# Kernel optimization log

Hardware: AMD Instinct MI355X
Metric: run time of the kernel (lower is better)

Reference implementation:

```python
import jax, jax.numpy as jnp
import numpy as np

B, H, S, D = 2, 16, 2048, 64
DEGREE = 2
EPS = 1e-4


def setup_inputs() -> dict:
    key = jax.random.key(0)
    kq, kk, kv = jax.random.split(key, 3)
    q = jax.random.normal(kq, (B, H, S, D), dtype=jnp.float32)
    k = jax.random.normal(kk, (B, H, S, D), dtype=jnp.float32)
    v = jax.random.normal(kv, (B, H, S, D), dtype=jnp.float32)
    return {"q": q, "k": k, "v": v}


def reference(q, k, v):
    # dots: [B,H,S,S] = QK^T
    dots = jnp.einsum("bhsd,bhtd->bhst", q, k)
    # polynomial kernel: x^degree, row-normalized with clamped denom
    x = dots ** DEGREE
    denom = jnp.maximum(x.sum(axis=-1, keepdims=True), EPS)
    attn = x / denom
    # weighted V sum: [B,H,S,D]
    return jnp.einsum("bhst,bhtd->bhsd", attn, v)
```

## Files before the change

### kernel.cpp

```cpp
#include <hip/hip_runtime.h>


#define S_LEN 2048
#define DH    64
#define BQ    64
#define BK    64
#define EPSTR 68
#define PSTR  65
#define BH_N  32
#define PER_BH (S_LEN * DH)
#define NT    (S_LEN / BK)

typedef __bf16 bf16x8 __attribute__((ext_vector_type(8)));
typedef __bf16 bf16x2 __attribute__((ext_vector_type(2)));
typedef float  f32x2  __attribute__((ext_vector_type(2)));
typedef float  f32x4  __attribute__((ext_vector_type(4)));
typedef float  f32x16 __attribute__((ext_vector_type(16)));
typedef unsigned int uivec2 __attribute__((ext_vector_type(2)));

__device__ __forceinline__ unsigned short f2bf(float f) {
    union { float f; unsigned int u; } x; x.f = f;
    unsigned int u = x.u;
    return (unsigned short)((u + 0x7fffu + ((u >> 16) & 1u)) >> 16);
}

__device__ __forceinline__ unsigned int pack2bf(float lo, float hi) {
#if __has_builtin(__builtin_amdgcn_cvt_pk_bf16_f32)
    bf16x2 p = __builtin_amdgcn_cvt_pk_bf16_f32(lo, hi);
    union { bf16x2 v; unsigned int u; } c; c.v = p;
    return c.u;
#else
    return (unsigned int)f2bf(lo) | ((unsigned int)f2bf(hi) << 16);
#endif
}

__device__ __forceinline__ void pl32swap(unsigned int& a, unsigned int& b) {
#if __has_builtin(__builtin_amdgcn_permlane32_swap)
    uivec2 r = __builtin_amdgcn_permlane32_swap(a, b, false, false);
    a = r[0]; b = r[1];
#else
    asm("v_permlane32_swap_b32 %0, %1" : "+v"(a), "+v"(b));
#endif
}

__global__ __launch_bounds__(256)
void prepass_kernel(const float* __restrict__ kg, const float* __restrict__ vg,
                    unsigned short* __restrict__ kfo, unsigned short* __restrict__ vfo)
{
    __shared__ unsigned short Lk[64 * 72];
    __shared__ unsigned short Lv[64 * PSTR];
    const int tid = threadIdx.x;
    const int bh  = blockIdx.y;
    const int t   = blockIdx.x;
    const size_t base = (size_t)bh * PER_BH + (size_t)t * 64 * DH;

    const float4* kf4 = (const float4*)(kg + base);
    const float4* vf4 = (const float4*)(vg + base);
    #pragma unroll
    for (int r = 0; r < 4; ++r) {
        int idx = r * 256 + tid;
        int row = idx >> 4, c4 = idx & 15;
        float4 f = kf4[idx];
        ushort4 hh;
        hh.x = f2bf(f.x); hh.y = f2bf(f.y); hh.z = f2bf(f.z); hh.w = f2bf(f.w);
        *(ushort4*)&Lk[row * 72 + c4 * 4] = hh;
        float4 g = vf4[idx];
        unsigned short* pv = &Lv[row * PSTR + c4 * 4];
        pv[0] = f2bf(g.x); pv[1] = f2bf(g.y); pv[2] = f2bf(g.z); pv[3] = f2bf(g.w);
    }
    __syncthreads();

    unsigned short* kout = kfo + (size_t)bh * PER_BH + (size_t)t * 4096;
    #pragma unroll
    for (int r = 0; r < 2; ++r) {
        int pos = r * 256 + tid;
        int lam = pos & 63, rest = pos >> 6;
        int e = rest >> 2, ks = rest & 3;
        int l31 = lam & 31, h = lam >> 5;
        uint4 v = *(const uint4*)&Lk[(e * 32 + l31) * 72 + ks * 16 + h * 8];
        *(uint4*)(kout + (size_t)pos * 8) = v;
    }
    unsigned short* vout = vfo + (size_t)bh * PER_BH + (size_t)t * 4096;
    #pragma unroll
    for (int r = 0; r < 2; ++r) {
        int pos = r * 256 + tid;
        int lam = pos & 63, rest = pos >> 6;
        int e = rest >> 2, ksl = (rest >> 1) & 1, mt = rest & 1;
        int l31 = lam & 31, h = lam >> 5;
        int d  = mt * 32 + l31;
        int j0 = e * 32 + ksl * 16 + h * 8;
        union { unsigned short s[8]; uint4 u; } u;
        #pragma unroll
        for (int jj = 0; jj < 8; ++jj) u.s[jj] = Lv[(j0 + jj) * PSTR + d];
        *(uint4*)(vout + (size_t)pos * 8) = u.u;
    }
}

__global__ __launch_bounds__(256, 3)
void poly_attn_main(const float* __restrict__ qg,
                    const unsigned short* __restrict__ kfo,
                    const unsigned short* __restrict__ vfo,
                    float* __restrict__ og)
{
    __shared__ float epb[4 * 32 * EPSTR];
    __shared__ float dbuf[128];

    const int tid  = threadIdx.x;
    const int lane = tid & 63;
    const int w    = tid >> 6;
    const int sp   = w >> 1;
    const int e    = w & 1;
    const int l31  = lane & 31;
    const int h    = lane >> 5;

    const int id = blockIdx.x;
    const int r5 = id & 31;
    const int bh = (r5 & 7) * 4 + (r5 >> 3);
    const int qt = id >> 5;
    const int q0 = qt * BQ;

    const float* qb = qg + ((size_t)bh * S_LEN + q0) * DH;
    const unsigned short* kw = kfo + (size_t)bh * PER_BH + e * 2048 + (size_t)lane * 8;
    const unsigned short* vw = vfo + (size_t)bh * PER_BH + e * 2048 + (size_t)lane * 8;
    float* ob = og + ((size_t)bh * S_LEN + q0) * DH;

    bf16x8 qfrag[4];
    #pragma unroll
    for (int ks = 0; ks < 4; ++ks) {
        const float* qp = qb + (32 * sp + l31) * DH + ks * 16 + h * 8;
        float4 f0 = *(const float4*)qp;
        float4 f1 = *(const float4*)(qp + 4);
        union { unsigned int d[4]; bf16x8 v; } u;
        u.d[0] = pack2bf(f0.x, f0.y);
        u.d[1] = pack2bf(f0.z, f0.w);
        u.d[2] = pack2bf(f1.x, f1.y);
        u.d[3] = pack2bf(f1.z, f1.w);
        qfrag[ks] = u.v;
    }

    f32x16 oacc[2];
    #pragma unroll
    for (int mt = 0; mt < 2; ++mt)
        #pragma unroll
        for (int r = 0; r < 16; ++r) oacc[mt][r] = 0.f;
    f32x16 oaccD;
    #pragma unroll
    for (int r = 0; r < 16; ++r) oaccD[r] = 0.f;

    f32x16 zacc;
    #pragma unroll
    for (int r = 0; r < 16; ++r) zacc[r] = 0.f;
    asm volatile("" : "+v"(zacc));

    bf16x8 onesv;
    {
        union { unsigned int d[4]; bf16x8 v; } u;
        u.d[0] = 0x3f803f80u; u.d[1] = 0x3f803f80u;
        u.d[2] = 0x3f803f80u; u.d[3] = 0x3f803f80u;
        onesv = u.v;
    }
    asm volatile("" : "+v"(onesv));

    uint4 kbuf[2][4], vbuf[4];
    unsigned int bsv[2][4];

    #pragma unroll
    for (int x = 0; x < 4; ++x) kbuf[0][x] = *(const uint4*)(kw + x * 512);

#define BODY(TT, CUR, NXT, KPF)                                                     \
    {                                                                               \
        {                                                                           \
            const unsigned short* vn_ = vw + (size_t)(TT) * 4096;                   \
            _Pragma("unroll")                                                       \
            for (int x = 0; x < 4; ++x) vbuf[x] = *(const uint4*)(vn_ + x * 512);   \
        }                                                                           \
        f32x16 acc;                                                                 \
        __builtin_amdgcn_s_setprio(1);                                              \
        {                                                                           \
            union { uint4 u; bf16x8 v; } kc;                                        \
            kc.u = kbuf[CUR][0];                                                    \
            acc = __builtin_amdgcn_mfma_f32_32x32x16_bf16(kc.v, qfrag[0], zacc, 0, 0, 0); \
            kc.u = kbuf[CUR][1];                                                    \
            acc = __builtin_amdgcn_mfma_f32_32x32x16_bf16(kc.v, qfrag[1], acc, 0, 0, 0); \
            kc.u = kbuf[CUR][2];                                                    \
            acc = __builtin_amdgcn_mfma_f32_32x32x16_bf16(kc.v, qfrag[2], acc, 0, 0, 0); \
            kc.u = kbuf[CUR][3];                                                    \
            acc = __builtin_amdgcn_mfma_f32_32x32x16_bf16(kc.v, qfrag[3], acc, 0, 0, 0); \
        }                                                                           \
        __builtin_amdgcn_s_setprio(0);                                              \
        if (KPF) {                                                                  \
            const unsigned short* kn_ = kw + (size_t)((TT) + 1) * 4096;             \
            _Pragma("unroll")                                                       \
            for (int x = 0; x < 4; ++x) kbuf[NXT][x] = *(const uint4*)(kn_ + x * 512); \
        }                                                                           \
        _Pragma("unroll")                                                           \
        for (int ksl = 0; ksl < 2; ++ksl) {                                         \
            f32x2 va, vb, vc, vd;                                                   \
            va[0] = acc[8*ksl+0]; va[1] = acc[8*ksl+1];                             \
            vb[0] = acc[8*ksl+2]; vb[1] = acc[8*ksl+3];                             \
            vc[0] = acc[8*ksl+4]; vc[1] = acc[8*ksl+5];                             \
            vd[0] = acc[8*ksl+6]; vd[1] = acc[8*ksl+7];                             \
            va = va * va; vb = vb * vb; vc = vc * vc; vd = vd * vd;                 \
            unsigned int a0 = pack2bf(va[0], va[1]);                                \
            unsigned int a1 = pack2bf(vb[0], vb[1]);                                \
            unsigned int b0 = pack2bf(vc[0], vc[1]);                                \
            unsigned int b1 = pack2bf(vd[0], vd[1]);                                \
            pl32swap(a0, b0);                                                       \
            pl32swap(a1, b1);                                                       \
            bsv[ksl][0] = a0; bsv[ksl][1] = a1;                                     \
            bsv[ksl][2] = b0; bsv[ksl][3] = b1;                                     \
        }                                                                           \
        __builtin_amdgcn_s_setprio(1);                                              \
        _Pragma("unroll")                                                           \
        for (int ksl = 0; ksl < 2; ++ksl) {                                         \
            union { unsigned int d[4]; bf16x8 v; } bu;                              \
            bu.d[0] = bsv[ksl][0]; bu.d[1] = bsv[ksl][1];                           \
            bu.d[2] = bsv[ksl][2]; bu.d[3] = bsv[ksl][3];                           \
            union { uint4 u; bf16x8 v; } vv;                                        \
            vv.u = vbuf[ksl * 2 + 0];                                               \
            oacc[0] = __builtin_amdgcn_mfma_f32_32x32x16_bf16(vv.v, bu.v, oacc[0], 0, 0, 0); \
            vv.u = vbuf[ksl * 2 + 1];                                               \
            oacc[1] = __builtin_amdgcn_mfma_f32_32x32x16_bf16(vv.v, bu.v, oacc[1], 0, 0, 0); \
            oaccD  = __builtin_amdgcn_mfma_f32_32x32x16_bf16(onesv, bu.v, oaccD, 0, 0, 0); \
        }                                                                           \
        __builtin_amdgcn_s_setprio(0);                                              \
    }

    for (int T = 0; T < NT - 2; T += 2) {
        BODY(T,     0, 1, 1);
        BODY(T + 1, 1, 0, 1);
    }
    BODY(NT - 2, 0, 1, 1);
    BODY(NT - 1, 1, 0, 0);
#undef BODY

    const float wavetot = oaccD[0];

    {
        float* ep = epb + (size_t)w * (32 * EPSTR);
        #pragma unroll
        for (int mt = 0; mt < 2; ++mt) {
            #pragma unroll
            for (int g = 0; g < 4; ++g) {
                f32x4 vv;
                vv[0] = oacc[mt][4*g+0];
                vv[1] = oacc[mt][4*g+1];
                vv[2] = oacc[mt][4*g+2];
                vv[3] = oacc[mt][4*g+3];
                *(f32x4*)&ep[l31 * EPSTR + mt * 32 + 8 * g + 4 * h] = vv;
            }
        }
        if (h == 0) dbuf[w * 32 + l31] = wavetot;
    }
    __syncthreads();

    const int so = w >> 1, ho = w & 1;
    const int lr = lane >> 1;
    const float den = dbuf[(2 * so + 0) * 32 + lr] + dbuf[(2 * so + 1) * 32 + lr];
    const float inv = 1.0f / fmaxf(den, 1e-4f);
    const float* ea = epb + (size_t)(2 * so + 0) * (32 * EPSTR) + lr * EPSTR;
    const float* eb = epb + (size_t)(2 * so + 1) * (32 * EPSTR) + lr * EPSTR;
    #pragma unroll
    for (int it = 0; it < 4; ++it) {
        int d0 = ho * 32 + (lane & 1) * 16 + it * 4;
        f32x4 a = *(const f32x4*)&ea[d0];
        f32x4 b = *(const f32x4*)&eb[d0];
        f32x4 sm;
        sm[0] = (a[0] + b[0]) * inv;
        sm[1] = (a[1] + b[1]) * inv;
        sm[2] = (a[2] + b[2]) * inv;
        sm[3] = (a[3] + b[3]) * inv;
        *(f32x4*)&ob[(32 * so + lr) * DH + d0] = sm;
    }
}

#define LSTR 72
__global__ __launch_bounds__(256, 2)
void poly_attn_fallback(const float* __restrict__ qg, const float* __restrict__ kg,
                        const float* __restrict__ vg, float* __restrict__ og)
{
    __shared__ unsigned short Qs[64 * LSTR];
    __shared__ unsigned short Ksl[64 * LSTR];
    __shared__ unsigned short Vt[64 * LSTR];
    __shared__ unsigned short Xsl[64 * LSTR];

    const int tid  = threadIdx.x;
    const int lane = tid & 63;
    const int w    = tid >> 6;
    const int c    = lane & 15;
    const int quad = lane >> 4;
    const int i0   = w * 16;

    const int bh = blockIdx.y;
    const int q0 = blockIdx.x * 64;

    const float* qb = qg + ((size_t)bh * S_LEN + q0) * DH;
    const float* kb = kg + (size_t)bh * S_LEN * DH;
    const float* vb = vg + (size_t)bh * S_LEN * DH;
    float*       ob = og + ((size_t)bh * S_LEN + q0) * DH;

    {
        const float4* qf4 = (const float4*)qb;
        #pragma unroll
        for (int r = 0; r < 4; ++r) {
            int idx = r * 256 + tid;
            int row = idx >> 4, c4 = idx & 15;
            float4 f = qf4[idx];
            ushort4 hh;
            hh.x = f2bf(f.x); hh.y = f2bf(f.y); hh.z = f2bf(f.z); hh.w = f2bf(f.w);
            *(ushort4*)&Qs[row * LSTR + c4 * 4] = hh;
        }
    }

    f32x4 oacc[4];
    #pragma unroll
    for (int t = 0; t < 4; ++t) { oacc[t][0]=0.f; oacc[t][1]=0.f; oacc[t][2]=0.f; oacc[t][3]=0.f; }
    float dsum[4] = {0.f, 0.f, 0.f, 0.f};

    for (int t0 = 0; t0 < S_LEN; t0 += 64) {
        __syncthreads();
        {
            const float4* kf4 = (const float4*)(kb + (size_t)t0 * DH);
            const float4* vf4 = (const float4*)(vb + (size_t)t0 * DH);
            #pragma unroll
            for (int r = 0; r < 4; ++r) {
                int idx = r * 256 + tid;
                int row = idx >> 4, c4 = idx & 15;
                float4 f = kf4[idx];
                ushort4 hh;
                hh.x = f2bf(f.x); hh.y = f2bf(f.y); hh.z = f2bf(f.z); hh.w = f2bf(f.w);
                *(ushort4*)&Ksl[row * LSTR + c4 * 4] = hh;
                float4 g = vf4[idx];
                int d0 = c4 * 4;
                Vt[(d0 + 0) * LSTR + row] = f2bf(g.x);
                Vt[(d0 + 1) * LSTR + row] = f2bf(g.y);
                Vt[(d0 + 2) * LSTR + row] = f2bf(g.z);
                Vt[(d0 + 3) * LSTR + row] = f2bf(g.w);
            }
        }
        __syncthreads();

        f32x4 xacc[4];
        #pragma unroll
        for (int t = 0; t < 4; ++t) { xacc[t][0]=0.f; xacc[t][1]=0.f; xacc[t][2]=0.f; xacc[t][3]=0.f; }
        #pragma unroll
        for (int k0 = 0; k0 < 64; k0 += 32) {
            bf16x8 af = *(const bf16x8*)&Qs[(i0 + c) * LSTR + k0 + quad * 8];
            #pragma unroll
            for (int tn = 0; tn < 4; ++tn) {
                bf16x8 bfg = *(const bf16x8*)&Ksl[(tn * 16 + c) * LSTR + k0 + quad * 8];
                xacc[tn] = __builtin_amdgcn_mfma_f32_16x16x32_bf16(af, bfg, xacc[tn], 0, 0, 0);
            }
        }
        #pragma unroll
        for (int tn = 0; tn < 4; ++tn)
            #pragma unroll
            for (int r = 0; r < 4; ++r) {
                float xv = xacc[tn][r];
                float xs = xv * xv;
                dsum[r] += xs;
                Xsl[(i0 + quad * 4 + r) * LSTR + tn * 16 + c] = f2bf(xs);
            }
        __syncthreads();

        #pragma unroll
        for (int k0 = 0; k0 < 64; k0 += 32) {
            bf16x8 af = *(const bf16x8*)&Xsl[(i0 + c) * LSTR + k0 + quad * 8];
            #pragma unroll
            for (int tn = 0; tn < 4; ++tn) {
                bf16x8 bfg = *(const bf16x8*)&Vt[(tn * 16 + c) * LSTR + k0 + quad * 8];
                oacc[tn] = __builtin_amdgcn_mfma_f32_16x16x32_bf16(af, bfg, oacc[tn], 0, 0, 0);
            }
        }
    }

    #pragma unroll
    for (int r = 0; r < 4; ++r) {
        float s = dsum[r];
        s += __shfl_xor(s, 1);
        s += __shfl_xor(s, 2);
        s += __shfl_xor(s, 4);
        s += __shfl_xor(s, 8);
        dsum[r] = 1.0f / fmaxf(s, 1e-4f);
    }
    #pragma unroll
    for (int tn = 0; tn < 4; ++tn)
        #pragma unroll
        for (int r = 0; r < 4; ++r)
            ob[(i0 + quad * 4 + r) * DH + tn * 16 + c] = oacc[tn][r] * dsum[r];
}

extern "C" void kernel_launch(void* const* d_in, const int* in_sizes, int n_in,
                              void* d_out, int out_size, void* d_ws, size_t ws_size,
                              hipStream_t stream) {
    (void)in_sizes; (void)n_in; (void)out_size;
    const float* q = (const float*)d_in[0];
    const float* k = (const float*)d_in[1];
    const float* v = (const float*)d_in[2];
    float* o = (float*)d_out;

    const size_t elems = (size_t)BH_N * PER_BH;
    const size_t need  = 2 * elems * sizeof(unsigned short);

    if (ws_size >= need) {
        unsigned short* kfo = (unsigned short*)d_ws;
        unsigned short* vfo = kfo + elems;
        prepass_kernel<<<dim3(NT, BH_N), 256, 0, stream>>>(k, v, kfo, vfo);
        poly_attn_main<<<dim3(BH_N * S_LEN / BQ), 256, 0, stream>>>(q, kfo, vfo, o);
    } else {
        poly_attn_fallback<<<dim3(S_LEN / 64, BH_N), 256, 0, stream>>>(q, k, v, o);
    }
}
```

Before: 143.1 us.

## Stage K/V tiles through LDS with async DMA and barrier-phased MFMA schedule

The main kernel now uses 512-thread blocks covering 128 query rows, so K/V tiles staged in shared memory are shared by twice as many waves. Tiles are loaded with global_load_lds DMA into a 4-slot ring, two tiles ahead. Each tile is split into barrier-separated phases that interleave LDS fragment reads with QK and PV MFMAs. The ones-vector MFMA used for the denominator is replaced by a VALU accumulation of squared scores plus a cross-half shuffle. This aims to cut redundant global K/V traffic and hide load latency, at the cost of many block-wide barriers per tile and about 69 KB of LDS per block, which limits occupancy.

```diff
diff --git a/kernel.cpp b/kernel.cpp
--- a/kernel.cpp
+++ b/kernel.cpp
@@ -3,13 +3,15 @@
 
 #define S_LEN 2048
 #define DH    64
-#define BQ    64
+#define BQ    128
 #define BK    64
 #define EPSTR 68
 #define PSTR  65
 #define BH_N  32
 #define PER_BH (S_LEN * DH)
 #define NT    (S_LEN / BK)
+#define SLOT  16384
+#define SMEM_BYTES 70656
 
 typedef __bf16 bf16x8 __attribute__((ext_vector_type(8)));
 typedef __bf16 bf16x2 __attribute__((ext_vector_type(2)));
@@ -41,6 +43,12 @@
 #else
     asm("v_permlane32_swap_b32 %0, %1" : "+v"(a), "+v"(b));
 #endif
+}
+
+__device__ __forceinline__ void dma16(const void* g, void* l) {
+    __builtin_amdgcn_global_load_lds(
+        (const __attribute__((address_space(1))) unsigned int*)g,
+        (__attribute__((address_space(3))) unsigned int*)l, 16, 0, 0);
 }
 
 __global__ __launch_bounds__(256)
@@ -96,14 +104,13 @@
     }
 }
 
-__global__ __launch_bounds__(256, 3)
+__global__ __launch_bounds__(512, 4)
 void poly_attn_main(const float* __restrict__ qg,
                     const unsigned short* __restrict__ kfo,
                     const unsigned short* __restrict__ vfo,
                     float* __restrict__ og)
 {
-    __shared__ float epb[4 * 32 * EPSTR];
-    __shared__ float dbuf[128];
+    __shared__ __align__(16) unsigned char smem[SMEM_BYTES];
 
     const int tid  = threadIdx.x;
     const int lane = tid & 63;
@@ -120,9 +127,15 @@
     const int q0 = qt * BQ;
 
     const float* qb = qg + ((size_t)bh * S_LEN + q0) * DH;
-    const unsigned short* kw = kfo + (size_t)bh * PER_BH + e * 2048 + (size_t)lane * 8;
-    const unsigned short* vw = vfo + (size_t)bh * PER_BH + e * 2048 + (size_t)lane * 8;
     float* ob = og + ((size_t)bh * S_LEN + q0) * DH;
+
+    const unsigned short* gkw = kfo + (size_t)bh * PER_BH + w * 512 + (size_t)lane * 8;
+    const unsigned short* gvw = vfo + (size_t)bh * PER_BH + w * 512 + (size_t)lane * 8;
+    unsigned char* ldsK = smem + w * 1024;
+    unsigned char* ldsV = smem + 8192 + w * 1024;
+
+    const unsigned char* rdK = smem + e * 4096 + (size_t)lane * 16;
+    const unsigned char* rdV = smem + 8192 + e * 4096 + (size_t)lane * 16;
 
     bf16x8 qfrag[4];
     #pragma unroll
@@ -137,105 +150,154 @@
         u.d[3] = pack2bf(f1.z, f1.w);
         qfrag[ks] = u.v;
     }
+    __builtin_amdgcn_sched_barrier(0);
 
     f32x16 oacc[2];
     #pragma unroll
     for (int mt = 0; mt < 2; ++mt)
         #pragma unroll
         for (int r = 0; r < 16; ++r) oacc[mt][r] = 0.f;
-    f32x16 oaccD;
-    #pragma unroll
-    for (int r = 0; r < 16; ++r) oaccD[r] = 0.f;
+    f32x2 ds2; ds2[0] = 0.f; ds2[1] = 0.f;
 
     f32x16 zacc;
     #pragma unroll
     for (int r = 0; r < 16; ++r) zacc[r] = 0.f;
     asm volatile("" : "+v"(zacc));
 
-    bf16x8 onesv;
-    {
-        union { unsigned int d[4]; bf16x8 v; } u;
-        u.d[0] = 0x3f803f80u; u.d[1] = 0x3f803f80u;
-        u.d[2] = 0x3f803f80u; u.d[3] = 0x3f803f80u;
-        onesv = u.v;
-    }
-    asm volatile("" : "+v"(onesv));
-
-    uint4 kbuf[2][4], vbuf[4];
+    uint4 kfr0, kfr1, kfr2, kfr3, vfr0, vfr1, vfp2, vfp3;
+    f32x16 acc;
     unsigned int bsv[2][4];
 
-    #pragma unroll
-    for (int x = 0; x < 4; ++x) kbuf[0][x] = *(const uint4*)(kw + x * 512);
-
-#define BODY(TT, CUR, NXT, KPF)                                                     \
+#define WAITVM_(N) asm volatile("s_waitcnt vmcnt(" #N ")" ::: "memory")
+#define WAITVM(N) WAITVM_(N)
+#define LGKM0 asm volatile("s_waitcnt lgkmcnt(0)" ::: "memory")
+#define BARR  __builtin_amdgcn_s_barrier()
+#define SB0   __builtin_amdgcn_sched_barrier(0)
+#define PRIO1 __builtin_amdgcn_s_setprio(1)
+#define PRIO0 __builtin_amdgcn_s_setprio(0)
+
+#define XF_STAGE()                                                                  \
     {                                                                               \
-        {                                                                           \
-            const unsigned short* vn_ = vw + (size_t)(TT) * 4096;                   \
-            _Pragma("unroll")                                                       \
-            for (int x = 0; x < 4; ++x) vbuf[x] = *(const uint4*)(vn_ + x * 512);   \
-        }                                                                           \
-        f32x16 acc;                                                                 \
-        __builtin_amdgcn_s_setprio(1);                                              \
-        {                                                                           \
-            union { uint4 u; bf16x8 v; } kc;                                        \
-            kc.u = kbuf[CUR][0];                                                    \
-            acc = __builtin_amdgcn_mfma_f32_32x32x16_bf16(kc.v, qfrag[0], zacc, 0, 0, 0); \
-            kc.u = kbuf[CUR][1];                                                    \
-            acc = __builtin_amdgcn_mfma_f32_32x32x16_bf16(kc.v, qfrag[1], acc, 0, 0, 0); \
-            kc.u = kbuf[CUR][2];                                                    \
-            acc = __builtin_amdgcn_mfma_f32_32x32x16_bf16(kc.v, qfrag[2], acc, 0, 0, 0); \
-            kc.u = kbuf[CUR][3];                                                    \
-            acc = __builtin_amdgcn_mfma_f32_32x32x16_bf16(kc.v, qfrag[3], acc, 0, 0, 0); \
-        }                                                                           \
-        __builtin_amdgcn_s_setprio(0);                                              \
-        if (KPF) {                                                                  \
-            const unsigned short* kn_ = kw + (size_t)((TT) + 1) * 4096;             \
-            _Pragma("unroll")                                                       \
-            for (int x = 0; x < 4; ++x) kbuf[NXT][x] = *(const uint4*)(kn_ + x * 512); \
+        unsigned int pk[4][2];                                                      \
+        _Pragma("unroll")                                                           \
+        for (int g = 0; g < 4; ++g) {                                               \
+            f32x2 v01, v23;                                                         \
+            v01[0] = acc[4*g+0]; v01[1] = acc[4*g+1];                               \
+            v23[0] = acc[4*g+2]; v23[1] = acc[4*g+3];                               \
+            v01 = v01 * v01; v23 = v23 * v23;                                       \
+            ds2 += v01; ds2 += v23;                                                 \
+            pk[g][0] = pack2bf(v01[0], v01[1]);                                     \
+            pk[g][1] = pack2bf(v23[0], v23[1]);                                     \
         }                                                                           \
         _Pragma("unroll")                                                           \
         for (int ksl = 0; ksl < 2; ++ksl) {                                         \
-            f32x2 va, vb, vc, vd;                                                   \
-            va[0] = acc[8*ksl+0]; va[1] = acc[8*ksl+1];                             \
-            vb[0] = acc[8*ksl+2]; vb[1] = acc[8*ksl+3];                             \
-            vc[0] = acc[8*ksl+4]; vc[1] = acc[8*ksl+5];                             \
-            vd[0] = acc[8*ksl+6]; vd[1] = acc[8*ksl+7];                             \
-            va = va * va; vb = vb * vb; vc = vc * vc; vd = vd * vd;                 \
-            unsigned int a0 = pack2bf(va[0], va[1]);                                \
-            unsigned int a1 = pack2bf(vb[0], vb[1]);                                \
-            unsigned int b0 = pack2bf(vc[0], vc[1]);                                \
-            unsigned int b1 = pack2bf(vd[0], vd[1]);                                \
+            unsigned int a0 = pk[2*ksl][0], b0 = pk[2*ksl+1][0];                    \
+            unsigned int a1 = pk[2*ksl][1], b1 = pk[2*ksl+1][1];                    \
             pl32swap(a0, b0);                                                       \
             pl32swap(a1, b1);                                                       \
             bsv[ksl][0] = a0; bsv[ksl][1] = a1;                                     \
             bsv[ksl][2] = b0; bsv[ksl][3] = b1;                                     \
         }                                                                           \
-        __builtin_amdgcn_s_setprio(1);                                              \
-        _Pragma("unroll")                                                           \
-        for (int ksl = 0; ksl < 2; ++ksl) {                                         \
+    }
+
+#define TILE(TT, DODMA, VMC, DOPVB)                                                 \
+    {                                                                               \
+        const size_t so_ = (size_t)((TT) & 3) * SLOT;                               \
+                      \
+        kfr0 = *(const uint4*)(rdK + so_);                                          \
+        kfr1 = *(const uint4*)(rdK + so_ + 1024);                                   \
+        if (DODMA) {                                                                \
+            const size_t go_ = (size_t)((TT) + 2) * 4096;                           \
+            const size_t sn_ = (size_t)(((TT) + 2) & 3) * SLOT;                     \
+            dma16(gkw + go_, ldsK + sn_);                                           \
+            dma16(gvw + go_, ldsV + sn_);                                           \
+        }                                                                           \
+        BARR; LGKM0; SB0; PRIO1;                                                    \
+        if (DOPVB) {                                                                \
             union { unsigned int d[4]; bf16x8 v; } bu;                              \
-            bu.d[0] = bsv[ksl][0]; bu.d[1] = bsv[ksl][1];                           \
-            bu.d[2] = bsv[ksl][2]; bu.d[3] = bsv[ksl][3];                           \
+            bu.d[0] = bsv[1][0]; bu.d[1] = bsv[1][1];                               \
+            bu.d[2] = bsv[1][2]; bu.d[3] = bsv[1][3];                               \
             union { uint4 u; bf16x8 v; } vv;                                        \
-            vv.u = vbuf[ksl * 2 + 0];                                               \
+            vv.u = vfp2;                                                            \
             oacc[0] = __builtin_amdgcn_mfma_f32_32x32x16_bf16(vv.v, bu.v, oacc[0], 0, 0, 0); \
-            vv.u = vbuf[ksl * 2 + 1];                                               \
+            vv.u = vfp3;                                                            \
             oacc[1] = __builtin_amdgcn_mfma_f32_32x32x16_bf16(vv.v, bu.v, oacc[1], 0, 0, 0); \
-            oaccD  = __builtin_amdgcn_mfma_f32_32x32x16_bf16(onesv, bu.v, oaccD, 0, 0, 0); \
-        }                                                                           \
-        __builtin_amdgcn_s_setprio(0);                                              \
-    }
-
-    for (int T = 0; T < NT - 2; T += 2) {
-        BODY(T,     0, 1, 1);
-        BODY(T + 1, 1, 0, 1);
-    }
-    BODY(NT - 2, 0, 1, 1);
-    BODY(NT - 1, 1, 0, 0);
-#undef BODY
-
-    const float wavetot = oaccD[0];
-
+        }                                                                           \
+        PRIO0; BARR;                                                                \
+                                            \
+        kfr2 = *(const uint4*)(rdK + so_ + 2048);                                   \
+        kfr3 = *(const uint4*)(rdK + so_ + 3072);                                   \
+        BARR; LGKM0; SB0; PRIO1;                                                    \
+        {                                                                           \
+            union { uint4 u; bf16x8 v; } kc;                                        \
+            kc.u = kfr0;                                                            \
+            acc = __builtin_amdgcn_mfma_f32_32x32x16_bf16(kc.v, qfrag[0], zacc, 0, 0, 0); \
+            kc.u = kfr1;                                                            \
+            acc = __builtin_amdgcn_mfma_f32_32x32x16_bf16(kc.v, qfrag[1], acc, 0, 0, 0); \
+        }                                                                           \
+        PRIO0; BARR;                                                                \
+                                            \
+        vfr0 = *(const uint4*)(rdV + so_);                                          \
+        vfr1 = *(const uint4*)(rdV + so_ + 1024);                                   \
+        BARR; LGKM0; SB0; PRIO1;                                                    \
+        {                                                                           \
+            union { uint4 u; bf16x8 v; } kc;                                        \
+            kc.u = kfr2;                                                            \
+            acc = __builtin_amdgcn_mfma_f32_32x32x16_bf16(kc.v, qfrag[2], acc, 0, 0, 0); \
+            kc.u = kfr3;                                                            \
+            acc = __builtin_amdgcn_mfma_f32_32x32x16_bf16(kc.v, qfrag[3], acc, 0, 0, 0); \
+        }                                                                           \
+        PRIO0; BARR;                                                                \
+                             \
+        vfp2 = *(const uint4*)(rdV + so_ + 2048);                                   \
+        vfp3 = *(const uint4*)(rdV + so_ + 3072);                                   \
+        XF_STAGE();                                                                 \
+        WAITVM(VMC);                                                                \
+        BARR; LGKM0; SB0; PRIO1;                                                    \
+        {                                                                           \
+            union { unsigned int d[4]; bf16x8 v; } bu;                              \
+            bu.d[0] = bsv[0][0]; bu.d[1] = bsv[0][1];                               \
+            bu.d[2] = bsv[0][2]; bu.d[3] = bsv[0][3];                               \
+            union { uint4 u; bf16x8 v; } vv;                                        \
+            vv.u = vfr0;                                                            \
+            oacc[0] = __builtin_amdgcn_mfma_f32_32x32x16_bf16(vv.v, bu.v, oacc[0], 0, 0, 0); \
+            vv.u = vfr1;                                                            \
+            oacc[1] = __builtin_amdgcn_mfma_f32_32x32x16_bf16(vv.v, bu.v, oacc[1], 0, 0, 0); \
+        }                                                                           \
+        PRIO0; BARR;                                                                \
+    }
+
+    dma16(gkw, ldsK);
+    dma16(gvw, ldsV);
+    dma16(gkw + 4096, ldsK + SLOT);
+    dma16(gvw + 4096, ldsV + SLOT);
+    WAITVM(2);
+    BARR;
+
+    TILE(0, 1, 2, 0)
+    for (int T = 1; T <= 29; ++T) {
+        TILE(T, 1, 2, 1)
+    }
+    TILE(30, 0, 0, 1)
+    TILE(31, 0, 0, 1)
+    {
+        union { unsigned int d[4]; bf16x8 v; } bu;
+        bu.d[0] = bsv[1][0]; bu.d[1] = bsv[1][1];
+        bu.d[2] = bsv[1][2]; bu.d[3] = bsv[1][3];
+        union { uint4 u; bf16x8 v; } vv;
+        vv.u = vfp2;
+        oacc[0] = __builtin_amdgcn_mfma_f32_32x32x16_bf16(vv.v, bu.v, oacc[0], 0, 0, 0);
+        vv.u = vfp3;
+        oacc[1] = __builtin_amdgcn_mfma_f32_32x32x16_bf16(vv.v, bu.v, oacc[1], 0, 0, 0);
+    }
+#undef TILE
+#undef XF_STAGE
+
+    float wavetot;
+    { float t = ds2[0] + ds2[1]; wavetot = t + __shfl_xor(t, 32); }
+
+    float* epb  = (float*)smem;
+    float* dbuf = (float*)(smem + 69632);
     {
         float* ep = epb + (size_t)w * (32 * EPSTR);
         #pragma unroll
@@ -254,23 +316,28 @@
     }
     __syncthreads();
 
-    const int so = w >> 1, ho = w & 1;
-    const int lr = lane >> 1;
-    const float den = dbuf[(2 * so + 0) * 32 + lr] + dbuf[(2 * so + 1) * 32 + lr];
-    const float inv = 1.0f / fmaxf(den, 1e-4f);
-    const float* ea = epb + (size_t)(2 * so + 0) * (32 * EPSTR) + lr * EPSTR;
-    const float* eb = epb + (size_t)(2 * so + 1) * (32 * EPSTR) + lr * EPSTR;
-    #pragma unroll
-    for (int it = 0; it < 4; ++it) {
-        int d0 = ho * 32 + (lane & 1) * 16 + it * 4;
-        f32x4 a = *(const f32x4*)&ea[d0];
-        f32x4 b = *(const f32x4*)&eb[d0];
-        f32x4 sm;
-        sm[0] = (a[0] + b[0]) * inv;
-        sm[1] = (a[1] + b[1]) * inv;
-        sm[2] = (a[2] + b[2]) * inv;
-        sm[3] = (a[3] + b[3]) * inv;
-        *(f32x4*)&ob[(32 * so + lr) * DH + d0] = sm;
+    {
+        const int lr   = lane >> 2;
+        const int quad = lane & 3;
+        const int r    = 16 * w + lr;
+        const int S    = r >> 5;
+        const int i    = r & 31;
+        const float den = dbuf[(2 * S + 0) * 32 + i] + dbuf[(2 * S + 1) * 32 + i];
+        const float inv = 1.0f / fmaxf(den, 1e-4f);
+        const float* ea = epb + (size_t)(2 * S + 0) * (32 * EPSTR) + i * EPSTR;
+        const float* eb = epb + (size_t)(2 * S + 1) * (32 * EPSTR) + i * EPSTR;
+        #pragma unroll
+        for (int it = 0; it < 4; ++it) {
+            int d0 = quad * 16 + it * 4;
+            f32x4 a = *(const f32x4*)&ea[d0];
+            f32x4 b = *(const f32x4*)&eb[d0];
+            f32x4 sm;
+            sm[0] = (a[0] + b[0]) * inv;
+            sm[1] = (a[1] + b[1]) * inv;
+            sm[2] = (a[2] + b[2]) * inv;
+            sm[3] = (a[3] + b[3]) * inv;
+            *(f32x4*)&ob[(size_t)r * DH + d0] = sm;
+        }
     }
 }
 
@@ -406,7 +473,7 @@
         unsigned short* kfo = (unsigned short*)d_ws;
         unsigned short* vfo = kfo + elems;
         prepass_kernel<<<dim3(NT, BH_N), 256, 0, stream>>>(k, v, kfo, vfo);
-        poly_attn_main<<<dim3(BH_N * S_LEN / BQ), 256, 0, stream>>>(q, kfo, vfo, o);
+        poly_attn_main<<<dim3(BH_N * S_LEN / BQ), 512, 0, stream>>>(q, kfo, vfo, o);
     } else {
         poly_attn_fallback<<<dim3(S_LEN / 64, BH_N), 256, 0, stream>>>(q, k, v, o);
     }
```

Measured after the change: 144.2 us. No clear change (+0.7%).
